# Kernel tuning notes

Hardware: AMD Instinct MI355X
Metric: run time of the kernel (lower is better)

The kernel has to match this reference:

```python
import jax, jax.numpy as jnp
import numpy as np
import math

B, L, D = 8, 2048, 768
ORDER, EMB = 128, 5
FFT = 2 * L
MIN_DECAY = math.log(0.01) / 1.5   # slow_decay_pct = 1.5
MAX_DECAY = math.log(0.01) / 0.3   # fast_decay_pct = 0.3
SHIFT = 0.0


def _pos_emb(seq_len, emb_dim):
    # pos_emb_init from the source: [t, Re(z), Im(z)] with bands = (emb_dim-1)//2
    bands = (emb_dim - 1) // 2
    t = jnp.linspace(0.0, 1.0, seq_len)[None, :, None]
    t_res = jnp.linspace(0.0, seq_len - 1, seq_len)[None, :, None]
    w = 2.0 * jnp.pi * t_res / seq_len
    f = jnp.linspace(1e-4, bands - 1, bands)[None, None]
    zc = jnp.exp(-1j * f * w)
    return jnp.concatenate([t, zc.real, zc.imag], axis=-1).astype(jnp.float32)  # (1, L, EMB)


def setup_inputs() -> dict:
    key = jax.random.key(0)
    ks = jax.random.split(key, 16)
    s = 0.02
    return {
        "u": jax.random.normal(ks[0], (B, L, D), jnp.float32),
        "in_W": jax.random.normal(ks[1], (D, 3 * D), jnp.float32) * s,
        "in_b": jnp.zeros((3 * D,), jnp.float32),
        "out_W": jax.random.normal(ks[2], (D, D), jnp.float32) * s,
        "out_b": jnp.zeros((D,), jnp.float32),
        "x1_s": jax.random.normal(ks[3], (D, 4), jnp.float32) * 0.25,
        "x2_s": jax.random.normal(ks[4], (D, 4), jnp.float32) * 0.25,
        "v_s": jax.random.normal(ks[5], (D, 4), jnp.float32) * 0.25,
        "x1_sb": jax.random.normal(ks[6], (D,), jnp.float32) * 0.1,
        "x2_sb": jax.random.normal(ks[7], (D,), jnp.float32) * 0.1,
        "v_sb": jax.random.normal(ks[8], (D,), jnp.float32) * 0.1,
        "D_bias": jax.random.normal(ks[9], (D,), jnp.float32),
        "z": _pos_emb(L, EMB),
        "sin_freq": 10.0 * jnp.ones((1, ORDER), jnp.float32),   # hyena_w = 10
        "eo_mat": jax.random.normal(ks[10], (1, EMB, ORDER), jnp.float32) * 0.3,
        "eo_bias": jnp.zeros((1, ORDER), jnp.float32),
        "oo1_mat": jax.random.normal(ks[11], (1, ORDER, ORDER), jnp.float32) * 0.08,
        "oo1_bias": jnp.zeros((1, ORDER), jnp.float32),
        "oo2_mat": jax.random.normal(ks[12], (1, ORDER, ORDER), jnp.float32) * 0.08,
        "oo2_bias": jnp.zeros((1, ORDER), jnp.float32),
        "oh_mat": jax.random.normal(ks[13], (1, ORDER, D), jnp.float32) * 0.08,
    }


def _depthwise4(x, w, b):
    # torch Conv1d(groups=3D, kernel=4, padding=3) truncated to [:L] == causal conv, left pad 3
    out = jax.lax.conv_general_dilated(
        x, w[:, None, :], window_strides=(1,), padding=[(3, 0)],
        dimension_numbers=("NCH", "OIH", "NCH"), feature_group_count=x.shape[1])
    return out + b[None, :, None]


def _hyena_filter(z, sin_freq, eo_mat, eo_bias, oo1_mat, oo1_bias, oo2_mat, oo2_bias, oh_mat):
    # then exponential decay modulation (exp_mod_in_place_fwd), channels=1, reverse=0.
    f = sin_freq[:, None, :]                                       # (1, 1, ORDER)
    h = jnp.sin(f * (jnp.einsum("cle,ceo->clo", z, eo_mat) + eo_bias[:, None, :]))
    h = jnp.sin(f * (jnp.einsum("clo,cop->clp", h, oo1_mat) + oo1_bias[:, None, :]))
    h = jnp.sin(f * (jnp.einsum("clo,cop->clp", h, oo2_mat) + oo2_bias[:, None, :]))
    k = jnp.einsum("clo,coh->clh", h, oh_mat)                      # (1, L, D)
    t = jnp.linspace(0.0, 1.0, k.shape[1])
    deltas = jnp.abs(jnp.linspace(MIN_DECAY, MAX_DECAY, k.shape[2]))
    k = k * (jnp.exp(-t[None, :, None] * deltas[None, None, :]) + SHIFT)
    return k[0].T                                                  # (D, L)


def _forward(u, in_W, in_b, out_W, out_b, x1_s, x2_s, v_s, x1_sb, x2_sb, v_sb,
             D_bias, z, sin_freq, eo_mat, eo_bias, oo1_mat, oo1_bias,
             oo2_mat, oo2_bias, oh_mat):
    seqlen = u.shape[1]
    k = _hyena_filter(z, sin_freq, eo_mat, eo_bias, oo1_mat, oo1_bias, oo2_mat, oo2_bias, oh_mat)
    x1x2v = u @ in_W + in_b                                        # (B, L, 3D)
    x1, x2, v = jnp.split(x1x2v, 3, axis=-1)
    x1 = jnp.transpose(x1, (0, 2, 1))                              # (B, D, L)
    x2 = jnp.transpose(x2, (0, 2, 1))
    v = jnp.transpose(v, (0, 2, 1))
    x1 = _depthwise4(x1, x1_s, x1_sb)
    x2 = _depthwise4(x2, x2_s, x2_sb)
    v = _depthwise4(v, v_s, v_sb)
    v = v * x1                                                     # first gate
    k_f = jnp.fft.rfft(k.astype(jnp.float32), n=FFT)               # (D, FFT//2+1)
    v_f = jnp.fft.rfft(v.astype(jnp.float32), n=FFT)               # (B, D, FFT//2+1)
    y = jnp.fft.irfft(v_f * k_f[None], n=FFT)[..., :seqlen]        # long FFT conv
    y = y + v * D_bias[None, :, None]                              # skip term
    y = y * x2                                                     # second gate
    y = jnp.transpose(y, (0, 2, 1))                                # (B, L, D)
    return y @ out_W + out_b


def reference(u, in_W, in_b, out_W, out_b, x1_s, x2_s, v_s, x1_sb, x2_sb, v_sb,
              D_bias, z, sin_freq, eo_mat, eo_bias, oo1_mat, oo1_bias,
              oo2_mat, oo2_bias, oh_mat):
    return _forward(u, in_W, in_b, out_W, out_b, x1_s, x2_s, v_s, x1_sb, x2_sb, v_sb,
                    D_bias, z, sin_freq, eo_mat, eo_bias, oo1_mat, oo1_bias,
                    oo2_mat, oo2_bias, oh_mat)
```

## Files before the change

### kernel.cpp

```cpp
#include <hip/hip_runtime.h>


typedef __bf16 bf16x8 __attribute__((ext_vector_type(8)));
typedef float  f32x4  __attribute__((ext_vector_type(4)));

#define AS1 __attribute__((address_space(1)))
#define AS3 __attribute__((address_space(3)))
#define GLD16(gp, lp) __builtin_amdgcn_global_load_lds((AS1 void*)(void*)(gp), (AS3 void*)(void*)(lp), 16, 0, 0)

#define LGKM_BAR       __asm__ __volatile__("s_waitcnt lgkmcnt(0)\n\ts_barrier" ::: "memory")
#define VM_LGKM_BAR(N) __asm__ __volatile__("s_waitcnt vmcnt(" #N ") lgkmcnt(0)\n\ts_barrier" ::: "memory")

__device__ __forceinline__ unsigned short f2b(float f) {
    unsigned u = __builtin_bit_cast(unsigned, f);
    unsigned r = (u + 0x7fffu + ((u >> 16) & 1u)) >> 16;
    return (unsigned short)r;
}
__device__ __forceinline__ float b2f(unsigned short h) {
    unsigned u = ((unsigned)h) << 16;
    return __builtin_bit_cast(float, u);
}
__device__ __forceinline__ float b2f_lo(unsigned u) {
    return __builtin_bit_cast(float, u << 16);
}
__device__ __forceinline__ float b2f_hi(unsigned u) {
    return __builtin_bit_cast(float, u & 0xffff0000u);
}

__device__ __forceinline__ float2 cmul(float2 a, float2 b) {
    return make_float2(a.x * b.x - a.y * b.y, a.x * b.y + a.y * b.x);
}
__device__ __forceinline__ float2 cmulc(float2 a, float2 b) {
    return make_float2(a.x * b.x + a.y * b.y, a.y * b.x - a.x * b.y);
}
__device__ __forceinline__ float2 cadd(float2 a, float2 b) { return make_float2(a.x + b.x, a.y + b.y); }
__device__ __forceinline__ float2 csub(float2 a, float2 b) { return make_float2(a.x - b.x, a.y - b.y); }

#define TWO_PI 6.283185307179586f
__device__ float2 d_Tw1[4096];
__device__ float2 d_Tw2[256];

__global__ __launch_bounds__(256) void twiddle_init_kernel() {
    const int i = blockIdx.x * 256 + threadIdx.x;
    if (i < 4096) {
        const int tt = i >> 4, k = i & 15;
        float s, c;
        __sincosf(-(float)(tt * k) * (TWO_PI / 4096.0f), &s, &c);
        d_Tw1[i] = make_float2(c, s);
    } else {
        const int j = i - 4096;
        const int lo = j >> 4, k = j & 15;
        float s, c;
        __sincosf(-(float)(lo * k) * (TWO_PI / 256.0f), &s, &c);
        d_Tw2[j] = make_float2(c, s);
    }
}

#define BFLY(i,j)   { float2 ta=x[i], tb=x[j]; x[i]=cadd(ta,tb); x[j]=csub(ta,tb); }
#define BFLYW(i,j,w){ float2 ta=x[i], tb=x[j]; x[i]=cadd(ta,tb); x[j]=cmul(csub(ta,tb),(w)); }
#define BFLYI(i,j)  { float2 ta=x[i], tb=x[j]; x[i]=cadd(ta,tb); float2 tt=csub(ta,tb); x[j]=make_float2(-dd*tt.y, dd*tt.x); }
#define CSWAP(i,j)  { float2 tt=x[i]; x[i]=x[j]; x[j]=tt; }

template<int DIR, bool UZ>
__device__ __forceinline__ void dft16(float2* x) {
    const float dd = (float)DIR;
    const float C1 = 0.92387953251128674f, S1 = 0.38268343236508977f, R2 = 0.70710678118654752f;
    const float2 W1 = make_float2( C1, dd*S1);
    const float2 W2 = make_float2( R2, dd*R2);
    const float2 W3 = make_float2( S1, dd*C1);
    const float2 W5 = make_float2(-S1, dd*C1);
    const float2 W6 = make_float2(-R2, dd*R2);
    const float2 W7 = make_float2(-C1, dd*S1);
    if (UZ) {
        x[8]  = x[0];
        x[9]  = cmul(x[1], W1);
        x[10] = cmul(x[2], W2);
        x[11] = cmul(x[3], W3);
        x[12] = make_float2(-dd*x[4].y, dd*x[4].x);
        x[13] = cmul(x[5], W5);
        x[14] = cmul(x[6], W6);
        x[15] = cmul(x[7], W7);
    } else {
        BFLY(0,8); BFLYW(1,9,W1); BFLYW(2,10,W2); BFLYW(3,11,W3);
        BFLYI(4,12); BFLYW(5,13,W5); BFLYW(6,14,W6); BFLYW(7,15,W7);
    }
    BFLY(0,4);  BFLYW(1,5,W2);  BFLYI(2,6);   BFLYW(3,7,W6);
    BFLY(8,12); BFLYW(9,13,W2); BFLYI(10,14); BFLYW(11,15,W6);
    BFLY(0,2);  BFLYI(1,3);  BFLY(4,6);   BFLYI(5,7);
    BFLY(8,10); BFLYI(9,11); BFLY(12,14); BFLYI(13,15);
    BFLY(0,1); BFLY(2,3); BFLY(4,5); BFLY(6,7);
    BFLY(8,9); BFLY(10,11); BFLY(12,13); BFLY(14,15);
    CSWAP(1,8); CSWAP(2,4); CSWAP(3,12); CSWAP(5,10); CSWAP(7,14); CSWAP(11,13);
}

__device__ __forceinline__ int ph1(int row, int col) { return row * 256 + (col ^ row); }
__device__ __forceinline__ int ph2(int row, int col) { return row * 16 + (col ^ (row & 15)); }

__device__ __forceinline__ void fft4096_fwd(float2* x, float2* lds, int t) {
    float2 w[16];
    #pragma unroll
    for (int k = 1; k < 16; ++k) w[k] = d_Tw1[t * 16 + k];
    dft16<-1, true>(x);
    #pragma unroll
    for (int k = 1; k < 16; ++k) x[k] = cmul(x[k], w[k]);
    #pragma unroll
    for (int k1 = 0; k1 < 16; ++k1) lds[ph1(k1, t)] = x[k1];
    __syncthreads();
    const int hi = t >> 4, lo = t & 15;
    #pragma unroll
    for (int t1 = 0; t1 < 16; ++t1) x[t1] = lds[ph1(hi, t1 * 16 + lo)];
    #pragma unroll
    for (int k = 1; k < 16; ++k) w[k] = d_Tw2[lo * 16 + k];
    dft16<-1, false>(x);
    #pragma unroll
    for (int k = 1; k < 16; ++k) x[k] = cmul(x[k], w[k]);
    __syncthreads();
    #pragma unroll
    for (int k2 = 0; k2 < 16; ++k2) lds[ph2(t, k2)] = x[k2];
    __syncthreads();
    #pragma unroll
    for (int t0 = 0; t0 < 16; ++t0) x[t0] = lds[ph2(hi * 16 + t0, lo)];
    dft16<-1, false>(x);
}

__device__ __forceinline__ void fft4096_inv(float2* x, float2* lds, int t) {
    const int hi = t >> 4, lo = t & 15;
    float2 w[16];
    dft16<1, false>(x);
    __syncthreads();
    #pragma unroll
    for (int t0 = 0; t0 < 16; ++t0) lds[ph2(hi * 16 + t0, lo)] = x[t0];
    #pragma unroll
    for (int k = 1; k < 16; ++k) w[k] = d_Tw2[lo * 16 + k];
    __syncthreads();
    #pragma unroll
    for (int k2 = 0; k2 < 16; ++k2) x[k2] = lds[ph2(t, k2)];
    #pragma unroll
    for (int k = 1; k < 16; ++k) x[k] = cmulc(x[k], w[k]);
    dft16<1, false>(x);
    __syncthreads();
    #pragma unroll
    for (int t1 = 0; t1 < 16; ++t1) lds[ph1(hi, t1 * 16 + lo)] = x[t1];
    #pragma unroll
    for (int k = 1; k < 16; ++k) w[k] = d_Tw1[t * 16 + k];
    __syncthreads();
    #pragma unroll
    for (int k1 = 0; k1 < 16; ++k1) x[k1] = lds[ph1(k1, t)];
    #pragma unroll
    for (int k = 1; k < 16; ++k) x[k] = cmulc(x[k], w[k]);
    dft16<1, false>(x);
}

__global__ __launch_bounds__(256) void filter_k_kernel(
    const float* __restrict__ z, const float* __restrict__ sf,
    const float* __restrict__ eo, const float* __restrict__ eo_b,
    const float* __restrict__ oo1, const float* __restrict__ oo1_b,
    const float* __restrict__ oo2, const float* __restrict__ oo2_b,
    const float* __restrict__ oh, float* __restrict__ kfil)
{
    __shared__ float h3buf[4][128];
    __shared__ float htmp[2][128];
    const int t = threadIdx.x;
    const int l0 = blockIdx.x * 4;
    const int half = t >> 7;
    const int o = t & 127;
    const float sfo = sf[o];
    for (int p = 0; p < 2; ++p) {
        const int li = p * 2 + half;
        const int l = l0 + li;
        float a = eo_b[o];
        #pragma unroll
        for (int e = 0; e < 5; ++e) a += z[l * 5 + e] * eo[e * 128 + o];
        htmp[half][o] = sinf(sfo * a);
        __syncthreads();
        float a2 = oo1_b[o];
        for (int q = 0; q < 128; ++q) a2 += htmp[half][q] * oo1[q * 128 + o];
        const float h2 = sinf(sfo * a2);
        __syncthreads();
        htmp[half][o] = h2;
        __syncthreads();
        float a3 = oo2_b[o];
        for (int q = 0; q < 128; ++q) a3 += htmp[half][q] * oo2[q * 128 + o];
        h3buf[li][o] = sinf(sfo * a3);
        __syncthreads();
    }
    const float MIND = -3.070113457325394f;
    const float MAXD = -15.350567286626972f;
    for (int c = 0; c < 3; ++c) {
        const int h = t + c * 256;
        float acc[4];
        #pragma unroll
        for (int li = 0; li < 4; ++li) acc[li] = 0.f;
        for (int q = 0; q < 128; ++q) {
            const float w = oh[q * 768 + h];
            #pragma unroll
            for (int li = 0; li < 4; ++li) acc[li] += h3buf[li][q] * w;
        }
        const float delta = fabsf(MIND + (MAXD - MIND) * (float)h * (1.0f / 767.0f));
        #pragma unroll
        for (int li = 0; li < 4; ++li) {
            const int l = l0 + li;
            const float tt = (float)l * (1.0f / 2047.0f);
            kfil[h * 2048 + l] = acc[li] * expf(-tt * delta);
        }
    }
}

__global__ __launch_bounds__(256) __attribute__((amdgpu_waves_per_eu(4, 5)))
void filter_fft_kernel(
    const float* __restrict__ kfil, float2* __restrict__ Kf)
{
    __shared__ __align__(16) float2 lds[4096];
    const int d = blockIdx.x, t = threadIdx.x;
    float2 x[16];
    #pragma unroll
    for (int r = 0; r < 8; ++r) x[r] = make_float2(kfil[d * 2048 + r * 256 + t], 0.f);
    fft4096_fwd(x, lds, t);
    const float s = 1.0f / 4096.0f;
    #pragma unroll
    for (int k3 = 0; k3 < 16; ++k3)
        Kf[d * 4096 + k3 * 256 + t] = make_float2(x[k3].x * s, x[k3].y * s);
}

__global__ __launch_bounds__(256) void convert_u_kernel(
    const float* __restrict__ u, unsigned short* __restrict__ ub)
{
    const int g = blockIdx.x * 256 + threadIdx.x;
    const float4 v = ((const float4*)u)[g];
    uint2 o;
    o.x = (unsigned)f2b(v.x) | ((unsigned)f2b(v.y) << 16);
    o.y = (unsigned)f2b(v.z) | ((unsigned)f2b(v.w) << 16);
    ((uint2*)ub)[g] = o;
}

__global__ __launch_bounds__(256) void transpose_W_kernel(
    const float* __restrict__ W, unsigned short* __restrict__ Wt, int K, int N)
{
    __shared__ float tile[32][33];
    const int n0 = blockIdx.x * 32, k0 = blockIdx.y * 32;
    const int tx = threadIdx.x & 31, ty = threadIdx.x >> 5;
    #pragma unroll
    for (int r = 0; r < 4; ++r) {
        const int kk = ty + r * 8;
        tile[kk][tx] = W[(k0 + kk) * N + n0 + tx];
    }
    __syncthreads();
    #pragma unroll
    for (int r = 0; r < 4; ++r) {
        const int nn = ty + r * 8;
        Wt[(n0 + nn) * K + k0 + tx] = f2b(tile[tx][nn]);
    }
}

__global__ __launch_bounds__(256) void transpose_Y_kernel(
    const unsigned short* __restrict__ Y, unsigned short* __restrict__ Yt)
{
    __shared__ unsigned short tile[32][34];
    const int bx = blockIdx.x;
    const int l0 = (bx & 63) * 32;
    const int tmp = bx >> 6;
    const int d0 = (tmp % 24) * 32;
    const int b  = tmp / 24;
    const int tx = threadIdx.x & 31, ty = threadIdx.x >> 5;
    #pragma unroll
    for (int r = 0; r < 4; ++r) {
        const int dd = ty + r * 8;
        tile[dd][tx] = Y[(b * 768 + d0 + dd) * 2048 + l0 + tx];
    }
    __syncthreads();
    #pragma unroll
    for (int r = 0; r < 4; ++r) {
        const int ll = ty + r * 8;
        Yt[(b * 2048 + l0 + ll) * 768 + d0 + tx] = tile[tx][ll];
    }
}

__global__ __launch_bounds__(512, 2) void gemm256_kernel(
    const unsigned short* __restrict__ A,
    const unsigned short* __restrict__ Bm,
    const float* __restrict__ bias,
    unsigned short* __restrict__ outb,
    float* __restrict__ outf,
    int mode)
{
    extern __shared__ __align__(16) unsigned short lds[];
    unsigned short* As = lds;
    unsigned short* Bs = lds + 32768;
    const int t = threadIdx.x;
    const int wv = t >> 6, lane = t & 63;
    const int row0 = (mode == 0 ? blockIdx.y : blockIdx.x) * 256;
    const int col0 = (mode == 0 ? blockIdx.x : blockIdx.y) * 256;
    const int wr = wv >> 2, wc = wv & 3;
    const int frow = lane & 15, kc = lane >> 4;

    f32x4 acc[8][4] = {};

    const int srow = t >> 3;
    const int cdat = (t & 7) ^ (srow & 7);
    const unsigned short* gA = A  + (row0 + srow) * 768 + cdat * 8;
    const unsigned short* gB = Bm + (col0 + srow) * 768 + cdat * 8;

#define STG_A(buf, q, koff) GLD16(gA + (q) * 49152 + (koff), (char*)As + (buf) * 32768 + (q) * 8192 + wv * 1024)
#define STG_B(buf, q, koff) GLD16(gB + (q) * 49152 + (koff), (char*)Bs + (buf) * 32768 + (q) * 8192 + wv * 1024)

    const int sx = frow & 7;
    const int aRowBase = (wr * 128 + frow) * 64;
    const int bRowBase = (wc * 64 + frow) * 64;
    const int sl0 = ((0 + kc) ^ sx) * 8;
    const int sl1 = ((4 + kc) ^ sx) * 8;

    bf16x8 aF[4][2], bN0[2][2], bN1[2][2];

#define READ_A(buf, mh)                                                         \
    _Pragma("unroll") for (int m = 0; m < 4; ++m) {                             \
        aF[m][0] = *(const bf16x8*)(As + (buf) * 16384 + aRowBase + ((mh) * 4 + m) * 1024 + sl0); \
        aF[m][1] = *(const bf16x8*)(As + (buf) * 16384 + aRowBase + ((mh) * 4 + m) * 1024 + sl1); \
    }
#define READ_B(buf, nh, arr)                                                    \
    _Pragma("unroll") for (int n = 0; n < 2; ++n) {                             \
        arr[n][0] = *(const bf16x8*)(Bs + (buf) * 16384 + bRowBase + ((nh) * 2 + n) * 1024 + sl0); \
        arr[n][1] = *(const bf16x8*)(Bs + (buf) * 16384 + bRowBase + ((nh) * 2 + n) * 1024 + sl1); \
    }
#define MFMA_Q(mh, nh, arr)                                                     \
    __builtin_amdgcn_s_setprio(1);                                              \
    _Pragma("unroll") for (int m = 0; m < 4; ++m)                               \
    _Pragma("unroll") for (int n = 0; n < 2; ++n)                               \
    _Pragma("unroll") for (int ks = 0; ks < 2; ++ks)                            \
        acc[(mh) * 4 + m][(nh) * 2 + n] = __builtin_amdgcn_mfma_f32_16x16x32_bf16( \
            aF[m][ks], arr[n][ks], acc[(mh) * 4 + m][(nh) * 2 + n], 0, 0, 0);   \
    __builtin_amdgcn_s_setprio(0);

    STG_A(0, 0, 0); STG_A(0, 1, 0); STG_A(0, 2, 0); STG_A(0, 3, 0);
    STG_B(0, 0, 0); STG_B(0, 1, 0); STG_B(0, 2, 0); STG_B(0, 3, 0);
    STG_A(1, 0, 64); STG_A(1, 2, 64);
    STG_B(1, 0, 64); STG_B(1, 1, 64); STG_B(1, 2, 64); STG_B(1, 3, 64);
    VM_LGKM_BAR(6);

    for (int i = 0; i < 5; ++i) {
        const int k1 = (2 * i + 1) * 64, k2 = (2 * i + 2) * 64, k3 = (2 * i + 3) * 64;
        READ_A(0, 0); READ_B(0, 0, bN0);
        STG_A(1, 1, k1); STG_A(1, 3, k1);
        MFMA_Q(0, 0, bN0);
        LGKM_BAR;
        READ_B(0, 1, bN1);
        STG_A(0, 0, k2); STG_A(0, 2, k2);
        MFMA_Q(0, 1, bN1);
        LGKM_BAR;
        READ_A(0, 1);
        STG_B(0, 0, k2); STG_B(0, 1, k2);
        MFMA_Q(1, 1, bN1);
        LGKM_BAR;
        STG_B(0, 2, k2); STG_B(0, 3, k2);
        MFMA_Q(1, 0, bN0);
        VM_LGKM_BAR(6);
        READ_A(1, 0); READ_B(1, 0, bN0);
        STG_A(0, 1, k2); STG_A(0, 3, k2);
        MFMA_Q(0, 0, bN0);
        LGKM_BAR;
        READ_B(1, 1, bN1);
        STG_A(1, 0, k3); STG_A(1, 2, k3);
        MFMA_Q(0, 1, bN1);
        LGKM_BAR;
        READ_A(1, 1);
        STG_B(1, 0, k3); STG_B(1, 1, k3);
        MFMA_Q(1, 1, bN1);
        LGKM_BAR;
        STG_B(1, 2, k3); STG_B(1, 3, k3);
        MFMA_Q(1, 0, bN0);
        VM_LGKM_BAR(6);
    }

    {
        READ_A(0, 0); READ_B(0, 0, bN0);
        STG_A(1, 1, 704); STG_A(1, 3, 704);
        MFMA_Q(0, 0, bN0);
        LGKM_BAR;
        READ_B(0, 1, bN1);
        MFMA_Q(0, 1, bN1);
        LGKM_BAR;
        READ_A(0, 1);
        MFMA_Q(1, 1, bN1);
        LGKM_BAR;
        MFMA_Q(1, 0, bN0);
        VM_LGKM_BAR(2);
        READ_A(1, 0); READ_B(1, 0, bN0);
        MFMA_Q(0, 0, bN0);
        LGKM_BAR;
        READ_B(1, 1, bN1);
        MFMA_Q(0, 1, bN1);
        VM_LGKM_BAR(0);
        READ_A(1, 1);
        MFMA_Q(1, 1, bN1);
        MFMA_Q(1, 0, bN0);
    }
#undef READ_A
#undef READ_B
#undef MFMA_Q
#undef STG_A
#undef STG_B

    if (mode == 0) {
        const int part = row0 / 768;
        const int bb = col0 / 2048;
        unsigned short* Xp = outb + (size_t)(part * 8 + bb) * 768 * 2048;
        const int drow0 = row0 - part * 768 + wr * 128 + (lane >> 4) * 4;
        const int lcol0 = col0 - bb * 2048 + wc * 64 + frow;
        #pragma unroll
        for (int m = 0; m < 8; ++m) {
            #pragma unroll
            for (int rr = 0; rr < 4; ++rr) {
                const int dd = drow0 + m * 16 + rr;
                const float bn = bias[row0 + wr * 128 + (lane >> 4) * 4 + m * 16 + rr];
                #pragma unroll
                for (int n = 0; n < 4; ++n)
                    Xp[dd * 2048 + lcol0 + n * 16] = f2b(acc[m][n][rr] + bn);
            }
        }
    } else {
        #pragma unroll
        for (int m = 0; m < 8; ++m) {
            #pragma unroll
            for (int rr = 0; rr < 4; ++rr) {
                const int mm = row0 + wr * 128 + (lane >> 4) * 4 + m * 16 + rr;
                #pragma unroll
                for (int n = 0; n < 4; ++n) {
                    const int nn = col0 + wc * 64 + n * 16 + frow;
                    outf[(size_t)mm * 768 + nn] = acc[m][n][rr] + bias[nn];
                }
            }
        }
    }
}

__device__ __forceinline__ void conv6(const unsigned short* __restrict__ p,
                                      const float* w, float bias, int t, float* out8)
{
    const uint4 m = *(const uint4*)(p + 8 * t);
    uint2 q = make_uint2(0u, 0u);
    if (t) q = *(const uint2*)(p + 8 * t - 4);
    float s[12];
    s[0] = b2f_lo(q.x); s[1] = b2f_hi(q.x); s[2] = b2f_lo(q.y); s[3] = b2f_hi(q.y);
    s[4] = b2f_lo(m.x); s[5] = b2f_hi(m.x); s[6] = b2f_lo(m.y); s[7] = b2f_hi(m.y);
    s[8] = b2f_lo(m.z); s[9] = b2f_hi(m.z); s[10] = b2f_lo(m.w); s[11] = b2f_hi(m.w);
    #pragma unroll
    for (int i = 0; i < 8; ++i)
        out8[i] = bias + w[0] * s[i + 1] + w[1] * s[i + 2] + w[2] * s[i + 3] + w[3] * s[i + 4];
}

__global__ __launch_bounds__(256) __attribute__((amdgpu_waves_per_eu(4, 4)))
void fft_conv_kernel(
    const unsigned short* __restrict__ X, const float2* __restrict__ Kf,
    const float* __restrict__ x1_s, const float* __restrict__ x2_s, const float* __restrict__ v_s,
    const float* __restrict__ x1_sb, const float* __restrict__ x2_sb, const float* __restrict__ v_sb,
    const float* __restrict__ D_bias, unsigned short* __restrict__ Y)
{
    __shared__ __align__(16) float2 lds[4096];
    unsigned* ldsu = (unsigned*)lds;
    const int d = blockIdx.x, jp = blockIdx.y, t = threadIdx.x;
    const int b0 = jp * 2, b1 = b0 + 1;

    float w1[4], w2[4], wv[4];
    #pragma unroll
    for (int j = 0; j < 4; ++j) { w1[j] = x1_s[d * 4 + j]; w2[j] = x2_s[d * 4 + j]; wv[j] = v_s[d * 4 + j]; }
    const float bc1 = x1_sb[d], bc2 = x2_sb[d], bcv = v_sb[d], Db = D_bias[d];

    const unsigned short* px1a = X + ((size_t)(0 * 8 + b0) * 768 + d) * 2048;
    const unsigned short* px2a = X + ((size_t)(1 * 8 + b0) * 768 + d) * 2048;
    const unsigned short* pva  = X + ((size_t)(2 * 8 + b0) * 768 + d) * 2048;
    const unsigned short* px1b = X + ((size_t)(0 * 8 + b1) * 768 + d) * 2048;
    const unsigned short* px2b = X + ((size_t)(1 * 8 + b1) * 768 + d) * 2048;
    const unsigned short* pvb  = X + ((size_t)(2 * 8 + b1) * 768 + d) * 2048;

    {
        float x1a[8], x2a[8], vva[8];
        conv6(px1a, w1, bc1, t, x1a);
        conv6(px2a, w2, bc2, t, x2a);
        conv6(pva,  wv, bcv, t, vva);
        float x1b[8], x2b[8], vvb[8];
        conv6(px1b, w1, bc1, t, x1b);
        conv6(px2b, w2, bc2, t, x2b);
        conv6(pvb,  wv, bcv, t, vvb);
        unsigned vh_pk[8], c2_pk[8];
        #pragma unroll
        for (int i = 0; i < 8; ++i) {
            vh_pk[i] = (unsigned)f2b(vva[i] * x1a[i]) | ((unsigned)f2b(vvb[i] * x1b[i]) << 16);
            c2_pk[i] = (unsigned)f2b(x2a[i]) | ((unsigned)f2b(x2b[i]) << 16);
        }
        *(uint4*)(ldsu + 8 * t)        = make_uint4(vh_pk[0], vh_pk[1], vh_pk[2], vh_pk[3]);
        *(uint4*)(ldsu + 8 * t + 4)    = make_uint4(vh_pk[4], vh_pk[5], vh_pk[6], vh_pk[7]);
        *(uint4*)(ldsu + 2048 + 8 * t)     = make_uint4(c2_pk[0], c2_pk[1], c2_pk[2], c2_pk[3]);
        *(uint4*)(ldsu + 2048 + 8 * t + 4) = make_uint4(c2_pk[4], c2_pk[5], c2_pk[6], c2_pk[7]);
    }
    __syncthreads();

    unsigned vhp[8], c2p[8];
    float2 x[16];
    #pragma unroll
    for (int r = 0; r < 8; ++r) {
        const unsigned u = ldsu[r * 256 + t];
        vhp[r] = u;
        x[r] = make_float2(b2f_lo(u), b2f_hi(u));
    }
    #pragma unroll
    for (int r = 0; r < 8; ++r) c2p[r] = ldsu[2048 + r * 256 + t];

    __syncthreads();

    fft4096_fwd(x, lds, t);

    {
        const float2* kf = Kf + (size_t)d * 4096;
        float2 kfr[16];
        #pragma unroll
        for (int k3 = 0; k3 < 16; ++k3) kfr[k3] = kf[k3 * 256 + t];
        #pragma unroll
        for (int k3 = 0; k3 < 16; ++k3) x[k3] = cmul(x[k3], kfr[k3]);
    }
    fft4096_inv(x, lds, t);

    unsigned short* ya = Y + ((size_t)b0 * 768 + d) * 2048;
    unsigned short* yb = Y + ((size_t)b1 * 768 + d) * 2048;
    #pragma unroll
    for (int n1 = 0; n1 < 8; ++n1) {
        const int l = n1 * 256 + t;
        const float va = b2f_lo(vhp[n1]);
        const float vb = b2f_hi(vhp[n1]);
        const float ca = b2f_lo(c2p[n1]);
        const float cb = b2f_hi(c2p[n1]);
        ya[l] = f2b((x[n1].x + va * Db) * ca);
        yb[l] = f2b((x[n1].y + vb * Db) * cb);
    }
}

extern "C" void kernel_launch(void* const* d_in, const int* in_sizes, int n_in,
                              void* d_out, int out_size, void* d_ws, size_t ws_size,
                              hipStream_t stream)
{
    (void)in_sizes; (void)n_in; (void)out_size; (void)ws_size;
    const float* u      = (const float*)d_in[0];
    const float* in_W   = (const float*)d_in[1];
    const float* in_b   = (const float*)d_in[2];
    const float* out_W  = (const float*)d_in[3];
    const float* out_b  = (const float*)d_in[4];
    const float* x1_s   = (const float*)d_in[5];
    const float* x2_s   = (const float*)d_in[6];
    const float* v_s    = (const float*)d_in[7];
    const float* x1_sb  = (const float*)d_in[8];
    const float* x2_sb  = (const float*)d_in[9];
    const float* v_sb   = (const float*)d_in[10];
    const float* D_bias = (const float*)d_in[11];
    const float* z      = (const float*)d_in[12];
    const float* sf     = (const float*)d_in[13];
    const float* eo     = (const float*)d_in[14];
    const float* eo_b   = (const float*)d_in[15];
    const float* oo1    = (const float*)d_in[16];
    const float* oo1_b  = (const float*)d_in[17];
    const float* oo2    = (const float*)d_in[18];
    const float* oo2_b  = (const float*)d_in[19];
    const float* oh     = (const float*)d_in[20];
    float* out = (float*)d_out;

    char* ws = (char*)d_ws;
    unsigned short* Xbf  = (unsigned short*)(ws + 0);
    unsigned short* Ybf  = (unsigned short*)(ws + 75497472);
    unsigned short* ubYt = (unsigned short*)(ws + 100663296);
    unsigned short* Wt   = (unsigned short*)(ws + 125829120);
    unsigned short* W2t  = (unsigned short*)(ws + 129368064);
    float*          kfil = (float*)(ws + 130547712);
    float2*         Kf   = (float2*)(ws + 136839168);

    static int attr_set = 0;
    if (!attr_set) {
        (void)hipFuncSetAttribute(reinterpret_cast<const void*>(gemm256_kernel),
                                  hipFuncAttributeMaxDynamicSharedMemorySize, 131072);
        attr_set = 1;
    }

    twiddle_init_kernel<<<17, 256, 0, stream>>>();
    filter_k_kernel<<<512, 256, 0, stream>>>(z, sf, eo, eo_b, oo1, oo1_b, oo2, oo2_b, oh, kfil);
    filter_fft_kernel<<<768, 256, 0, stream>>>(kfil, Kf);
    convert_u_kernel<<<12288, 256, 0, stream>>>(u, ubYt);
    transpose_W_kernel<<<dim3(72, 24), 256, 0, stream>>>(in_W, Wt, 768, 2304);
    transpose_W_kernel<<<dim3(24, 24), 256, 0, stream>>>(out_W, W2t, 768, 768);
    gemm256_kernel<<<dim3(64, 9), 512, 131072, stream>>>(Wt, ubYt, in_b, Xbf, nullptr, 0);
    fft_conv_kernel<<<dim3(768, 4), 256, 0, stream>>>(Xbf, Kf, x1_s, x2_s, v_s, x1_sb, x2_sb, v_sb, D_bias, Ybf);
    transpose_Y_kernel<<<12288, 256, 0, stream>>>(Ybf, ubYt);
    gemm256_kernel<<<dim3(64, 3), 512, 131072, stream>>>(ubYt, W2t, out_b, nullptr, out, 1);
}
```

Before: 428.4 us.

## Compute FFT twiddles on the fly, fold D skip into filter spectrum, defer x2 gate

Replaces the global twiddle tables and their init kernel with per-thread sincos plus power chains. The D_bias skip term is folded into the filter spectrum as a constant added to every frequency bin, which equals adding D*v in the time domain for the retained outputs. The x2 gate convolution is deferred until after the inverse FFT so it does not hold registers across the transforms. The kernel filter loads are chunked, and the waves_per_eu hints are dropped. Together these aim to cut register pressure and global loads, with some extra math and small precision risk from the recurrence-based twiddles.

```diff
diff --git a/kernel.cpp b/kernel.cpp
--- a/kernel.cpp
+++ b/kernel.cpp
@@ -16,10 +16,6 @@
     unsigned r = (u + 0x7fffu + ((u >> 16) & 1u)) >> 16;
     return (unsigned short)r;
 }
-__device__ __forceinline__ float b2f(unsigned short h) {
-    unsigned u = ((unsigned)h) << 16;
-    return __builtin_bit_cast(float, u);
-}
 __device__ __forceinline__ float b2f_lo(unsigned u) {
     return __builtin_bit_cast(float, u << 16);
 }
@@ -30,31 +26,10 @@
 __device__ __forceinline__ float2 cmul(float2 a, float2 b) {
     return make_float2(a.x * b.x - a.y * b.y, a.x * b.y + a.y * b.x);
 }
-__device__ __forceinline__ float2 cmulc(float2 a, float2 b) {
-    return make_float2(a.x * b.x + a.y * b.y, a.y * b.x - a.x * b.y);
-}
 __device__ __forceinline__ float2 cadd(float2 a, float2 b) { return make_float2(a.x + b.x, a.y + b.y); }
 __device__ __forceinline__ float2 csub(float2 a, float2 b) { return make_float2(a.x - b.x, a.y - b.y); }
 
 #define TWO_PI 6.283185307179586f
-__device__ float2 d_Tw1[4096];
-__device__ float2 d_Tw2[256];
-
-__global__ __launch_bounds__(256) void twiddle_init_kernel() {
-    const int i = blockIdx.x * 256 + threadIdx.x;
-    if (i < 4096) {
-        const int tt = i >> 4, k = i & 15;
-        float s, c;
-        __sincosf(-(float)(tt * k) * (TWO_PI / 4096.0f), &s, &c);
-        d_Tw1[i] = make_float2(c, s);
-    } else {
-        const int j = i - 4096;
-        const int lo = j >> 4, k = j & 15;
-        float s, c;
-        __sincosf(-(float)(lo * k) * (TWO_PI / 256.0f), &s, &c);
-        d_Tw2[j] = make_float2(c, s);
-    }
-}
 
 #define BFLY(i,j)   { float2 ta=x[i], tb=x[j]; x[i]=cadd(ta,tb); x[j]=csub(ta,tb); }
 #define BFLYW(i,j,w){ float2 ta=x[i], tb=x[j]; x[i]=cadd(ta,tb); x[j]=cmul(csub(ta,tb),(w)); }
@@ -93,27 +68,45 @@
     CSWAP(1,8); CSWAP(2,4); CSWAP(3,12); CSWAP(5,10); CSWAP(7,14); CSWAP(11,13);
 }
 
+__device__ __forceinline__ void twiddle16(float2* x, float ang) {
+    float s, c; __sincosf(ang, &s, &c);
+    const float2 u1  = make_float2(c, s);
+    const float2 u2  = cmul(u1, u1);
+    const float2 u3  = cmul(u2, u1);
+    const float2 u4  = cmul(u2, u2);
+    const float2 u8  = cmul(u4, u4);
+    const float2 u12 = cmul(u8, u4);
+    x[1]  = cmul(x[1],  u1);
+    x[2]  = cmul(x[2],  u2);
+    x[3]  = cmul(x[3],  u3);
+    x[4]  = cmul(x[4],  u4);
+    x[5]  = cmul(x[5],  cmul(u4, u1));
+    x[6]  = cmul(x[6],  cmul(u4, u2));
+    x[7]  = cmul(x[7],  cmul(u4, u3));
+    x[8]  = cmul(x[8],  u8);
+    x[9]  = cmul(x[9],  cmul(u8, u1));
+    x[10] = cmul(x[10], cmul(u8, u2));
+    x[11] = cmul(x[11], cmul(u8, u3));
+    x[12] = cmul(x[12], u12);
+    x[13] = cmul(x[13], cmul(u12, u1));
+    x[14] = cmul(x[14], cmul(u12, u2));
+    x[15] = cmul(x[15], cmul(u12, u3));
+}
+
 __device__ __forceinline__ int ph1(int row, int col) { return row * 256 + (col ^ row); }
 __device__ __forceinline__ int ph2(int row, int col) { return row * 16 + (col ^ (row & 15)); }
 
 __device__ __forceinline__ void fft4096_fwd(float2* x, float2* lds, int t) {
-    float2 w[16];
-    #pragma unroll
-    for (int k = 1; k < 16; ++k) w[k] = d_Tw1[t * 16 + k];
     dft16<-1, true>(x);
-    #pragma unroll
-    for (int k = 1; k < 16; ++k) x[k] = cmul(x[k], w[k]);
+    twiddle16(x, -(float)t * (TWO_PI / 4096.0f));
     #pragma unroll
     for (int k1 = 0; k1 < 16; ++k1) lds[ph1(k1, t)] = x[k1];
     __syncthreads();
     const int hi = t >> 4, lo = t & 15;
     #pragma unroll
     for (int t1 = 0; t1 < 16; ++t1) x[t1] = lds[ph1(hi, t1 * 16 + lo)];
-    #pragma unroll
-    for (int k = 1; k < 16; ++k) w[k] = d_Tw2[lo * 16 + k];
     dft16<-1, false>(x);
-    #pragma unroll
-    for (int k = 1; k < 16; ++k) x[k] = cmul(x[k], w[k]);
+    twiddle16(x, -(float)lo * (TWO_PI / 256.0f));
     __syncthreads();
     #pragma unroll
     for (int k2 = 0; k2 < 16; ++k2) lds[ph2(t, k2)] = x[k2];
@@ -125,29 +118,22 @@
 
 __device__ __forceinline__ void fft4096_inv(float2* x, float2* lds, int t) {
     const int hi = t >> 4, lo = t & 15;
-    float2 w[16];
     dft16<1, false>(x);
     __syncthreads();
     #pragma unroll
     for (int t0 = 0; t0 < 16; ++t0) lds[ph2(hi * 16 + t0, lo)] = x[t0];
-    #pragma unroll
-    for (int k = 1; k < 16; ++k) w[k] = d_Tw2[lo * 16 + k];
     __syncthreads();
     #pragma unroll
     for (int k2 = 0; k2 < 16; ++k2) x[k2] = lds[ph2(t, k2)];
-    #pragma unroll
-    for (int k = 1; k < 16; ++k) x[k] = cmulc(x[k], w[k]);
+    twiddle16(x, (float)lo * (TWO_PI / 256.0f));
     dft16<1, false>(x);
     __syncthreads();
     #pragma unroll
     for (int t1 = 0; t1 < 16; ++t1) lds[ph1(hi, t1 * 16 + lo)] = x[t1];
-    #pragma unroll
-    for (int k = 1; k < 16; ++k) w[k] = d_Tw1[t * 16 + k];
     __syncthreads();
     #pragma unroll
     for (int k1 = 0; k1 < 16; ++k1) x[k1] = lds[ph1(k1, t)];
-    #pragma unroll
-    for (int k = 1; k < 16; ++k) x[k] = cmulc(x[k], w[k]);
+    twiddle16(x, (float)t * (TWO_PI / 4096.0f));
     dft16<1, false>(x);
 }
 
@@ -206,9 +192,9 @@
     }
 }
 
-__global__ __launch_bounds__(256) __attribute__((amdgpu_waves_per_eu(4, 5)))
-void filter_fft_kernel(
-    const float* __restrict__ kfil, float2* __restrict__ Kf)
+__global__ __launch_bounds__(256) void filter_fft_kernel(
+    const float* __restrict__ kfil, const float* __restrict__ D_bias,
+    float2* __restrict__ Kf)
 {
     __shared__ __align__(16) float2 lds[4096];
     const int d = blockIdx.x, t = threadIdx.x;
@@ -216,10 +202,11 @@
     #pragma unroll
     for (int r = 0; r < 8; ++r) x[r] = make_float2(kfil[d * 2048 + r * 256 + t], 0.f);
     fft4096_fwd(x, lds, t);
+    const float db = D_bias[d];
     const float s = 1.0f / 4096.0f;
     #pragma unroll
     for (int k3 = 0; k3 < 16; ++k3)
-        Kf[d * 4096 + k3 * 256 + t] = make_float2(x[k3].x * s, x[k3].y * s);
+        Kf[d * 4096 + k3 * 256 + t] = make_float2((x[k3].x + db) * s, x[k3].y * s);
 }
 
 __global__ __launch_bounds__(256) void convert_u_kernel(
@@ -447,88 +434,102 @@
         out8[i] = bias + w[0] * s[i + 1] + w[1] * s[i + 2] + w[2] * s[i + 3] + w[3] * s[i + 4];
 }
 
-__global__ __launch_bounds__(256) __attribute__((amdgpu_waves_per_eu(4, 4)))
-void fft_conv_kernel(
+__global__ __launch_bounds__(256) void fft_conv_kernel(
     const unsigned short* __restrict__ X, const float2* __restrict__ Kf,
     const float* __restrict__ x1_s, const float* __restrict__ x2_s, const float* __restrict__ v_s,
     const float* __restrict__ x1_sb, const float* __restrict__ x2_sb, const float* __restrict__ v_sb,
-    const float* __restrict__ D_bias, unsigned short* __restrict__ Y)
+    unsigned short* __restrict__ Y)
 {
     __shared__ __align__(16) float2 lds[4096];
     unsigned* ldsu = (unsigned*)lds;
     const int d = blockIdx.x, jp = blockIdx.y, t = threadIdx.x;
     const int b0 = jp * 2, b1 = b0 + 1;
 
-    float w1[4], w2[4], wv[4];
-    #pragma unroll
-    for (int j = 0; j < 4; ++j) { w1[j] = x1_s[d * 4 + j]; w2[j] = x2_s[d * 4 + j]; wv[j] = v_s[d * 4 + j]; }
-    const float bc1 = x1_sb[d], bc2 = x2_sb[d], bcv = v_sb[d], Db = D_bias[d];
-
     const unsigned short* px1a = X + ((size_t)(0 * 8 + b0) * 768 + d) * 2048;
-    const unsigned short* px2a = X + ((size_t)(1 * 8 + b0) * 768 + d) * 2048;
     const unsigned short* pva  = X + ((size_t)(2 * 8 + b0) * 768 + d) * 2048;
     const unsigned short* px1b = X + ((size_t)(0 * 8 + b1) * 768 + d) * 2048;
-    const unsigned short* px2b = X + ((size_t)(1 * 8 + b1) * 768 + d) * 2048;
     const unsigned short* pvb  = X + ((size_t)(2 * 8 + b1) * 768 + d) * 2048;
 
     {
-        float x1a[8], x2a[8], vva[8];
-        conv6(px1a, w1, bc1, t, x1a);
-        conv6(px2a, w2, bc2, t, x2a);
-        conv6(pva,  wv, bcv, t, vva);
-        float x1b[8], x2b[8], vvb[8];
-        conv6(px1b, w1, bc1, t, x1b);
-        conv6(px2b, w2, bc2, t, x2b);
-        conv6(pvb,  wv, bcv, t, vvb);
-        unsigned vh_pk[8], c2_pk[8];
-        #pragma unroll
-        for (int i = 0; i < 8; ++i) {
-            vh_pk[i] = (unsigned)f2b(vva[i] * x1a[i]) | ((unsigned)f2b(vvb[i] * x1b[i]) << 16);
-            c2_pk[i] = (unsigned)f2b(x2a[i]) | ((unsigned)f2b(x2b[i]) << 16);
-        }
-        *(uint4*)(ldsu + 8 * t)        = make_uint4(vh_pk[0], vh_pk[1], vh_pk[2], vh_pk[3]);
-        *(uint4*)(ldsu + 8 * t + 4)    = make_uint4(vh_pk[4], vh_pk[5], vh_pk[6], vh_pk[7]);
-        *(uint4*)(ldsu + 2048 + 8 * t)     = make_uint4(c2_pk[0], c2_pk[1], c2_pk[2], c2_pk[3]);
-        *(uint4*)(ldsu + 2048 + 8 * t + 4) = make_uint4(c2_pk[4], c2_pk[5], c2_pk[6], c2_pk[7]);
-    }
-    __syncthreads();
-
-    unsigned vhp[8], c2p[8];
+        float w1[4], wv[4];
+        #pragma unroll
+        for (int j = 0; j < 4; ++j) { w1[j] = x1_s[d * 4 + j]; wv[j] = v_s[d * 4 + j]; }
+        const float bc1 = x1_sb[d], bcv = v_sb[d];
+        float pa[8];
+        {
+            float va[8], g[8];
+            conv6(pva,  wv, bcv, t, va);
+            conv6(px1a, w1, bc1, t, g);
+            #pragma unroll
+            for (int i = 0; i < 8; ++i) pa[i] = va[i] * g[i];
+        }
+        {
+            float vb[8], g[8];
+            conv6(pvb,  wv, bcv, t, vb);
+            conv6(px1b, w1, bc1, t, g);
+            unsigned vh[8];
+            #pragma unroll
+            for (int i = 0; i < 8; ++i)
+                vh[i] = (unsigned)f2b(pa[i]) | ((unsigned)f2b(vb[i] * g[i]) << 16);
+            *(uint4*)(ldsu + 8 * t)     = make_uint4(vh[0], vh[1], vh[2], vh[3]);
+            *(uint4*)(ldsu + 8 * t + 4) = make_uint4(vh[4], vh[5], vh[6], vh[7]);
+        }
+    }
+    __syncthreads();
+
     float2 x[16];
     #pragma unroll
     for (int r = 0; r < 8; ++r) {
         const unsigned u = ldsu[r * 256 + t];
-        vhp[r] = u;
         x[r] = make_float2(b2f_lo(u), b2f_hi(u));
     }
-    #pragma unroll
-    for (int r = 0; r < 8; ++r) c2p[r] = ldsu[2048 + r * 256 + t];
-
     __syncthreads();
 
     fft4096_fwd(x, lds, t);
 
     {
         const float2* kf = Kf + (size_t)d * 4096;
-        float2 kfr[16];
-        #pragma unroll
-        for (int k3 = 0; k3 < 16; ++k3) kfr[k3] = kf[k3 * 256 + t];
-        #pragma unroll
-        for (int k3 = 0; k3 < 16; ++k3) x[k3] = cmul(x[k3], kfr[k3]);
-    }
+        #pragma unroll
+        for (int c4 = 0; c4 < 4; ++c4) {
+            float2 kr[4];
+            #pragma unroll
+            for (int j = 0; j < 4; ++j) kr[j] = kf[(c4 * 4 + j) * 256 + t];
+            #pragma unroll
+            for (int j = 0; j < 4; ++j) x[c4 * 4 + j] = cmul(x[c4 * 4 + j], kr[j]);
+            __asm__ __volatile__("" ::: "memory");
+        }
+    }
+
     fft4096_inv(x, lds, t);
+
+    __syncthreads();
+    {
+        const unsigned short* px2a = X + ((size_t)(1 * 8 + b0) * 768 + d) * 2048;
+        const unsigned short* px2b = X + ((size_t)(1 * 8 + b1) * 768 + d) * 2048;
+        float w2[4];
+        #pragma unroll
+        for (int j = 0; j < 4; ++j) w2[j] = x2_s[d * 4 + j];
+        const float bc2 = x2_sb[d];
+        float ga[8], gb[8];
+        conv6(px2a, w2, bc2, t, ga);
+        conv6(px2b, w2, bc2, t, gb);
+        unsigned c2[8];
+        #pragma unroll
+        for (int i = 0; i < 8; ++i)
+            c2[i] = (unsigned)f2b(ga[i]) | ((unsigned)f2b(gb[i]) << 16);
+        *(uint4*)(ldsu + 8 * t)     = make_uint4(c2[0], c2[1], c2[2], c2[3]);
+        *(uint4*)(ldsu + 8 * t + 4) = make_uint4(c2[4], c2[5], c2[6], c2[7]);
+    }
+    __syncthreads();
 
     unsigned short* ya = Y + ((size_t)b0 * 768 + d) * 2048;
     unsigned short* yb = Y + ((size_t)b1 * 768 + d) * 2048;
     #pragma unroll
     for (int n1 = 0; n1 < 8; ++n1) {
         const int l = n1 * 256 + t;
-        const float va = b2f_lo(vhp[n1]);
-        const float vb = b2f_hi(vhp[n1]);
-        const float ca = b2f_lo(c2p[n1]);
-        const float cb = b2f_hi(c2p[n1]);
-        ya[l] = f2b((x[n1].x + va * Db) * ca);
-        yb[l] = f2b((x[n1].y + vb * Db) * cb);
+        const unsigned u = ldsu[l];
+        ya[l] = f2b(x[n1].x * b2f_lo(u));
+        yb[l] = f2b(x[n1].y * b2f_hi(u));
     }
 }
 
@@ -576,14 +577,13 @@
         attr_set = 1;
     }
 
-    twiddle_init_kernel<<<17, 256, 0, stream>>>();
     filter_k_kernel<<<512, 256, 0, stream>>>(z, sf, eo, eo_b, oo1, oo1_b, oo2, oo2_b, oh, kfil);
-    filter_fft_kernel<<<768, 256, 0, stream>>>(kfil, Kf);
+    filter_fft_kernel<<<768, 256, 0, stream>>>(kfil, D_bias, Kf);
     convert_u_kernel<<<12288, 256, 0, stream>>>(u, ubYt);
     transpose_W_kernel<<<dim3(72, 24), 256, 0, stream>>>(in_W, Wt, 768, 2304);
     transpose_W_kernel<<<dim3(24, 24), 256, 0, stream>>>(out_W, W2t, 768, 768);
     gemm256_kernel<<<dim3(64, 9), 512, 131072, stream>>>(Wt, ubYt, in_b, Xbf, nullptr, 0);
-    fft_conv_kernel<<<dim3(768, 4), 256, 0, stream>>>(Xbf, Kf, x1_s, x2_s, v_s, x1_sb, x2_sb, v_sb, D_bias, Ybf);
+    fft_conv_kernel<<<dim3(768, 4), 256, 0, stream>>>(Xbf, Kf, x1_s, x2_s, v_s, x1_sb, x2_sb, v_sb, Ybf);
     transpose_Y_kernel<<<12288, 256, 0, stream>>>(Ybf, ubYt);
     gemm256_kernel<<<dim3(64, 3), 512, 131072, stream>>>(ubYt, W2t, out_b, nullptr, out, 1);
 }
```

After: 361.6 us. 15.6% less time.
